# Optimization experiments

Hardware: AMD Instinct MI355X
Metric: run time of the kernel (lower is better)

Reference implementation:

```python
import jax, jax.numpy as jnp
import numpy as np

HID, HEADS, HD = 512, 8, 64  # hid_dim, n_heads, head_dim
NEG = -1e10


def setup_inputs() -> dict:
    key = jax.random.key(0)
    ks = jax.random.split(key, 12)
    B, S = 4, 2048
    inp = {
        'query': jax.random.normal(ks[0], (B, S, HID), jnp.float32),
        'key': jax.random.normal(ks[1], (B, S, HID), jnp.float32),
        'value': jax.random.normal(ks[2], (B, S, HID), jnp.float32),
        'mask': jnp.ones((B, 1, 1, S), jnp.int32),
    }
    sc = 1.0 / np.sqrt(HID)
    for i, n in enumerate(['Wq', 'Wk', 'Wv', 'Wo']):
        inp[n] = jax.random.uniform(ks[3 + i], (HID, HID), jnp.float32, -sc, sc)
    for i, n in enumerate(['bq', 'bk', 'bv', 'bo']):
        inp[n] = jax.random.uniform(ks[7 + i], (HID,), jnp.float32, -sc, sc)
    return inp


def reference(query, key, value, mask, Wq, Wk, Wv, Wo, bq, bk, bv, bo):
    B = query.shape[0]

    def proj(x, W, b):
        # torch Linear: x @ W.T + b; then split heads -> [B, H, S, HD]
        y = jnp.einsum('bsd,ed->bse', x, W) + b
        return y.reshape(B, -1, HEADS, HD).transpose(0, 2, 1, 3)

    Q = proj(query, Wq, bq)
    K = proj(key, Wk, bk)
    V = proj(value, Wv, bv)
    scale = jnp.sqrt(jnp.float32(HD))
    E = jnp.einsum('bhqd,bhkd->bhqk', Q, K) / scale  # [B,H,Sq,Sk]
    E = jnp.where(mask == 0, NEG, E)
    A = jax.nn.softmax(E, axis=-1)  # dropout p=0 -> identity
    out = jnp.einsum('bhqk,bhkd->bhqd', A, V)
    out = out.transpose(0, 2, 1, 3).reshape(B, -1, HID)
    return jnp.einsum('bsd,ed->bse', out, Wo) + bo
```

## Files before the change

kernel.cpp:

```cpp
#include <hip/hip_runtime.h>
#include <hip/hip_bf16.h>


typedef __bf16 v8bf __attribute__((ext_vector_type(8)));
typedef __bf16 v4bf __attribute__((ext_vector_type(4)));
typedef float  v4f  __attribute__((ext_vector_type(4)));

#define MFMA16(a, b, c) __builtin_amdgcn_mfma_f32_16x16x32_bf16((a), (b), (c), 0, 0, 0)

#define QSCALE 0.1803368801111f

__device__ inline v8bf cvt8(const float* __restrict__ p) {
    const v4f f0 = *(const v4f*)p;
    const v4f f1 = *(const v4f*)(p + 4);
    v8bf r;
    r[0] = (__bf16)f0[0]; r[1] = (__bf16)f0[1]; r[2] = (__bf16)f0[2]; r[3] = (__bf16)f0[3];
    r[4] = (__bf16)f1[0]; r[5] = (__bf16)f1[1]; r[6] = (__bf16)f1[2]; r[7] = (__bf16)f1[3];
    return r;
}

__global__ __launch_bounds__(256) void cvt_w(
    const float* __restrict__ Wq, const float* __restrict__ Wk,
    const float* __restrict__ Wv, const float* __restrict__ Wo,
    __bf16* __restrict__ out)
{
    const int idx = (blockIdx.x * 256 + threadIdx.x) * 4;
    const int w = idx >> 18, off = idx & 262143;
    const float* src = (w == 0) ? Wq : (w == 1) ? Wk : (w == 2) ? Wv : Wo;
    const float sc = (w == 0) ? QSCALE : 1.0f;
    const v4f x = *(const v4f*)(src + off);
    v4bf y;
    y[0] = (__bf16)(x[0] * sc); y[1] = (__bf16)(x[1] * sc);
    y[2] = (__bf16)(x[2] * sc); y[3] = (__bf16)(x[3] * sc);
    *(v4bf*)(out + idx) = y;
}

__global__ __launch_bounds__(256) void qkv_gemm(
    const float* __restrict__ xq, const float* __restrict__ xk, const float* __restrict__ xv,
    const __bf16* __restrict__ Wb,
    const float* __restrict__ bq, const float* __restrict__ bk, const float* __restrict__ bv,
    __bf16* __restrict__ Qo, __bf16* __restrict__ Ko, __bf16* __restrict__ VTo)
{
    const int z = blockIdx.z;
    const float*  x    = (z == 0) ? xq : (z == 1) ? xk : xv;
    const __bf16* W    = Wb + (size_t)z * 262144;
    const float*  bias = (z == 0) ? bq : (z == 1) ? bk : bv;
    const float   bsc  = (z == 0) ? QSCALE : 1.0f;

    const int tid = threadIdx.x, wave = tid >> 6, lane = tid & 63;
    const int quad = lane >> 4, r = lane & 15;
    const int wm = wave >> 1, wn = wave & 1;
    const int row0 = blockIdx.x * 128, col0 = blockIdx.y * 128;

    __shared__ __align__(16) __bf16 As[8192];
    __shared__ __align__(16) __bf16 Bs[8192];

    const float*  aptr[4];
    const __bf16* bptr[4];
    int adst[4], bdst[4];
    for (int j = 0; j < 4; j++) {
        const int e = tid + 256 * j;
        const int seg = e >> 6, ln = e & 63;
        aptr[j] = x + (size_t)(row0 + (seg >> 1) * 16 + (ln & 15)) * 512
                    + (seg & 1) * 32 + (ln >> 4) * 8;
        adst[j] = e * 8;
        const int segb = wave * 4 + j;
        bptr[j] = W + (size_t)(col0 + (segb >> 1) * 16 + r) * 512
                    + (segb & 1) * 32 + quad * 8;
        bdst[j] = (segb * 64 + lane) * 8;
    }

    v4f acc[4][4] = {};
    v8bf aReg[4], bReg[4];
    for (int j = 0; j < 4; j++) {
        aReg[j] = cvt8(aptr[j]);
        bReg[j] = *(const v8bf*)bptr[j];
    }

    for (int ki = 0; ki < 8; ki++) {
        __syncthreads();
        for (int j = 0; j < 4; j++) {
            *(v8bf*)&As[adst[j]] = aReg[j];
            *(v8bf*)&Bs[bdst[j]] = bReg[j];
        }
        __syncthreads();
        if (ki < 7) {
            const int kk = (ki + 1) * 64;
            for (int j = 0; j < 4; j++) {
                aReg[j] = cvt8(aptr[j] + kk);
                bReg[j] = *(const v8bf*)(bptr[j] + kk);
            }
        }
        for (int kc = 0; kc < 2; kc++) {
            v8bf a[4], b[4];
            for (int i = 0; i < 4; i++)
                a[i] = ((const v8bf*)As)[((wm * 4 + i) * 2 + kc) * 64 + lane];
            for (int i = 0; i < 4; i++)
                b[i] = ((const v8bf*)Bs)[((wn * 4 + i) * 2 + kc) * 64 + lane];
            for (int mi = 0; mi < 4; mi++)
                for (int ni = 0; ni < 4; ni++)
                    acc[mi][ni] = MFMA16(a[mi], b[ni], acc[mi][ni]);
        }
    }

    for (int ni = 0; ni < 4; ni++) {
        const int n = col0 + wn * 64 + ni * 16 + r;
        const float bv_ = bias[n] * bsc;
        const int hh = n >> 6, hd = n & 63;
        for (int mi = 0; mi < 4; mi++) {
            const int mbase = row0 + wm * 64 + mi * 16 + quad * 4;
            const int bb = mbase >> 11, s0 = mbase & 2047;
            if (z == 2) {
                v4bf pk;
                for (int i = 0; i < 4; i++)
                    pk[i] = (__bf16)(acc[mi][ni][i] + bv_);
                *(v4bf*)&VTo[((size_t)((bb * 8 + hh) * 64 + hd)) * 2048 + s0] = pk;
            } else {
                __bf16* dst = (z == 0) ? Qo : Ko;
                for (int i = 0; i < 4; i++)
                    dst[((size_t)((bb * 8 + hh) * 2048 + s0 + i)) * 64 + hd] =
                        (__bf16)(acc[mi][ni][i] + bv_);
            }
        }
    }
}

__global__ __launch_bounds__(256) void attn(
    const __bf16* __restrict__ Q, const __bf16* __restrict__ K,
    const __bf16* __restrict__ VT, const int* __restrict__ mask,
    __bf16* __restrict__ AO)
{
    const int bh = blockIdx.y, b = bh >> 3, h = bh & 7;
    const int tid = threadIdx.x, wave = tid >> 6, lane = tid & 63;
    const int quad = lane >> 4, r = lane & 15;
    const int q0 = blockIdx.x * 64 + wave * 16;

    const __bf16* Qb = Q  + (size_t)bh * 2048 * 64;
    const __bf16* Kb = K  + (size_t)bh * 2048 * 64;
    const __bf16* Vb = VT + (size_t)bh * 64 * 2048;
    const int*    mb = mask + (size_t)b * 2048;

    __shared__ __align__(16) __bf16 Kls[4096];
    __shared__ __align__(16) __bf16 Vls[4096];
    __shared__ __align__(16) __bf16 Pls[4][16][88];
    __shared__ __bf16 biasLS[2048];

    for (int i = tid; i < 2048; i += 256)
        biasLS[i] = (mb[i] != 0) ? (__bf16)0.f : (__bf16)(-1e10f);

    const int e1 = tid, e2 = tid + 256;
    int seg, l, t_, h_, rr, qd;
    seg = e1 >> 6; l = e1 & 63; t_ = seg >> 1; h_ = seg & 1; rr = l & 15; qd = l >> 4;
    const __bf16* kg1 = Kb + (size_t)(16 * t_ + rr) * 64   + h_ * 32 + qd * 8;
    const __bf16* vg1 = Vb + (size_t)(16 * t_ + rr) * 2048 + h_ * 32 + qd * 8;
    seg = e2 >> 6; l = e2 & 63; t_ = seg >> 1; h_ = seg & 1; rr = l & 15; qd = l >> 4;
    const __bf16* kg2 = Kb + (size_t)(16 * t_ + rr) * 64   + h_ * 32 + qd * 8;
    const __bf16* vg2 = Vb + (size_t)(16 * t_ + rr) * 2048 + h_ * 32 + qd * 8;

    v8bf qf0 = *(const v8bf*)(Qb + (size_t)(q0 + r) * 64 +      quad * 8);
    v8bf qf1 = *(const v8bf*)(Qb + (size_t)(q0 + r) * 64 + 32 + quad * 8);

    v8bf ones;
    for (int i = 0; i < 8; i++) ones[i] = (__bf16)1.0f;

    v4f o[4] = {};
    v4f lacc = {};

    v8bf ks1 = *(const v8bf*)kg1, ks2 = *(const v8bf*)kg2;
    v8bf vs1 = *(const v8bf*)vg1, vs2 = *(const v8bf*)vg2;

    for (int t = 0; t < 32; t++) {
        __syncthreads();
        ((v8bf*)Kls)[e1] = ks1; ((v8bf*)Kls)[e2] = ks2;
        ((v8bf*)Vls)[e1] = vs1; ((v8bf*)Vls)[e2] = vs2;
        __syncthreads();
        if (t < 31) {
            const int k0n = (t + 1) * 64;
            ks1 = *(const v8bf*)(kg1 + (size_t)k0n * 64);
            ks2 = *(const v8bf*)(kg2 + (size_t)k0n * 64);
            vs1 = *(const v8bf*)(vg1 + k0n);
            vs2 = *(const v8bf*)(vg2 + k0n);
        }
        const int k0 = t * 64;

        v4f sa[4] = {};
        for (int tt = 0; tt < 4; tt++) {
            v8bf kf0 = ((const v8bf*)Kls)[(tt * 2 + 0) * 64 + lane];
            v8bf kf1 = ((const v8bf*)Kls)[(tt * 2 + 1) * 64 + lane];
            sa[tt] = MFMA16(kf0, qf0, sa[tt]);
            sa[tt] = MFMA16(kf1, qf1, sa[tt]);
        }

        for (int tt = 0; tt < 4; tt++) {
            const v4bf bl = *(const v4bf*)&biasLS[k0 + tt * 16 + quad * 4];
            v4bf pk;
            for (int i = 0; i < 4; i++)
                pk[i] = (__bf16)exp2f(sa[tt][i] + (float)bl[i]);
            *(v4bf*)&Pls[wave][r][tt * 16 + quad * 4] = pk;
        }
        asm volatile("s_waitcnt lgkmcnt(0)" ::: "memory");
        v8bf pa0 = *(const v8bf*)&Pls[wave][r][     quad * 8];
        v8bf pa1 = *(const v8bf*)&Pls[wave][r][32 + quad * 8];

        lacc = MFMA16(pa0, ones, lacc);
        lacc = MFMA16(pa1, ones, lacc);

        for (int t2 = 0; t2 < 4; t2++) {
            v8bf vf0 = ((const v8bf*)Vls)[(t2 * 2 + 0) * 64 + lane];
            v8bf vf1 = ((const v8bf*)Vls)[(t2 * 2 + 1) * 64 + lane];
            o[t2] = MFMA16(pa0, vf0, o[t2]);
            o[t2] = MFMA16(pa1, vf1, o[t2]);
        }
    }

    for (int t2 = 0; t2 < 4; t2++) {
        const int hd = t2 * 16 + r;
        for (int i = 0; i < 4; i++) {
            const int s = q0 + quad * 4 + i;
            AO[((size_t)b * 2048 + s) * 512 + h * 64 + hd] = (__bf16)(o[t2][i] / lacc[i]);
        }
    }
}

__global__ __launch_bounds__(256) void out_gemm(
    const __bf16* __restrict__ Ai, const __bf16* __restrict__ W,
    const float* __restrict__ bias, float* __restrict__ y)
{
    const int tid = threadIdx.x, wave = tid >> 6, lane = tid & 63;
    const int quad = lane >> 4, r = lane & 15;
    const int wm = wave >> 1, wn = wave & 1;
    const int row0 = blockIdx.x * 128, col0 = blockIdx.y * 128;

    __shared__ __align__(16) __bf16 As[8192];
    __shared__ __align__(16) __bf16 Bs[8192];

    const __bf16* aptr[4];
    const __bf16* bptr[4];
    int dst_[4];
    for (int j = 0; j < 4; j++) {
        const int segb = wave * 4 + j;
        aptr[j] = Ai + (size_t)(row0 + (segb >> 1) * 16 + r) * 512 + (segb & 1) * 32 + quad * 8;
        bptr[j] = W  + (size_t)(col0 + (segb >> 1) * 16 + r) * 512 + (segb & 1) * 32 + quad * 8;
        dst_[j] = (segb * 64 + lane) * 8;
    }

    v4f acc[4][4] = {};
    v8bf aReg[4], bReg[4];
    for (int j = 0; j < 4; j++) {
        aReg[j] = *(const v8bf*)aptr[j];
        bReg[j] = *(const v8bf*)bptr[j];
    }

    for (int ki = 0; ki < 8; ki++) {
        __syncthreads();
        for (int j = 0; j < 4; j++) {
            *(v8bf*)&As[dst_[j]] = aReg[j];
            *(v8bf*)&Bs[dst_[j]] = bReg[j];
        }
        __syncthreads();
        if (ki < 7) {
            const int kk = (ki + 1) * 64;
            for (int j = 0; j < 4; j++) {
                aReg[j] = *(const v8bf*)(aptr[j] + kk);
                bReg[j] = *(const v8bf*)(bptr[j] + kk);
            }
        }
        for (int kc = 0; kc < 2; kc++) {
            v8bf a[4], b[4];
            for (int i = 0; i < 4; i++)
                a[i] = ((const v8bf*)As)[((wm * 4 + i) * 2 + kc) * 64 + lane];
            for (int i = 0; i < 4; i++)
                b[i] = ((const v8bf*)Bs)[((wn * 4 + i) * 2 + kc) * 64 + lane];
            for (int mi = 0; mi < 4; mi++)
                for (int ni = 0; ni < 4; ni++)
                    acc[mi][ni] = MFMA16(a[mi], b[ni], acc[mi][ni]);
        }
    }

    for (int ni = 0; ni < 4; ni++) {
        const int n = col0 + wn * 64 + ni * 16 + r;
        const float bv_ = bias[n];
        for (int mi = 0; mi < 4; mi++) {
            const int mbase = row0 + wm * 64 + mi * 16 + quad * 4;
            for (int i = 0; i < 4; i++)
                y[(size_t)(mbase + i) * 512 + n] = acc[mi][ni][i] + bv_;
        }
    }
}

extern "C" void kernel_launch(void* const* d_in, const int* in_sizes, int n_in,
                              void* d_out, int out_size, void* d_ws, size_t ws_size,
                              hipStream_t stream)
{
    const float* q    = (const float*)d_in[0];
    const float* k    = (const float*)d_in[1];
    const float* v    = (const float*)d_in[2];
    const int*   mask = (const int*)d_in[3];
    const float* Wq   = (const float*)d_in[4];
    const float* Wk   = (const float*)d_in[5];
    const float* Wv   = (const float*)d_in[6];
    const float* Wo   = (const float*)d_in[7];
    const float* bq   = (const float*)d_in[8];
    const float* bk   = (const float*)d_in[9];
    const float* bv   = (const float*)d_in[10];
    const float* bo   = (const float*)d_in[11];

    __bf16* ws  = (__bf16*)d_ws;
    __bf16* Qw  = ws;
    __bf16* Kw  = ws + 4194304;
    __bf16* VTw = ws + 8388608;
    __bf16* AOw = ws + 12582912;
    __bf16* Wb  = ws + 16777216;

    cvt_w<<<dim3(1024), 256, 0, stream>>>(Wq, Wk, Wv, Wo, Wb);
    qkv_gemm<<<dim3(64, 4, 3), 256, 0, stream>>>(q, k, v, Wb, bq, bk, bv, Qw, Kw, VTw);
    attn<<<dim3(32, 32), 256, 0, stream>>>(Qw, Kw, VTw, mask, AOw);
    out_gemm<<<dim3(64, 4), 256, 0, stream>>>(AOw, Wb + 786432, bo, (float*)d_out);
}
```

Measured before the change: 240.4 us.

## Keep attention probabilities in registers and feed PV via 16x16x16 MFMA

Drops the per-wave LDS round-trip for P: the S accumulator layout is reused directly as the B operand of a 16x16x16 bf16 MFMA against a padded V tile in LDS. The mask bias is folded into the QK MFMA accumulator init, and the row sum is computed with scalar adds plus cross-lane shuffles instead of an MFMA against a ones vector. The output is now stored as vectorized 4-wide bf16 writes. In exchange it uses twice as many smaller PV MFMAs and a new V staging layout with 72-element padding.

```diff
diff --git a/kernel.cpp b/kernel.cpp
--- a/kernel.cpp
+++ b/kernel.cpp
@@ -5,8 +5,14 @@
 typedef __bf16 v8bf __attribute__((ext_vector_type(8)));
 typedef __bf16 v4bf __attribute__((ext_vector_type(4)));
 typedef float  v4f  __attribute__((ext_vector_type(4)));
+typedef short  v4s  __attribute__((ext_vector_type(4)));
 
 #define MFMA16(a, b, c) __builtin_amdgcn_mfma_f32_16x16x32_bf16((a), (b), (c), 0, 0, 0)
+
+__device__ inline v4f MFMA_PV(v4bf a, v4bf b, v4f c) {
+    return __builtin_amdgcn_mfma_f32_16x16x16bf16_1k(
+        __builtin_bit_cast(v4s, a), __builtin_bit_cast(v4s, b), c, 0, 0, 0);
+}
 
 #define QSCALE 0.1803368801111f
 
@@ -141,38 +147,39 @@
     const int*    mb = mask + (size_t)b * 2048;
 
     __shared__ __align__(16) __bf16 Kls[4096];
-    __shared__ __align__(16) __bf16 Vls[4096];
-    __shared__ __align__(16) __bf16 Pls[4][16][88];
-    __shared__ __bf16 biasLS[2048];
+    __shared__ __align__(16) __bf16 Vls[64 * 72];
+    __shared__ float biasF[2048];
 
     for (int i = tid; i < 2048; i += 256)
-        biasLS[i] = (mb[i] != 0) ? (__bf16)0.f : (__bf16)(-1e10f);
+        biasF[i] = (mb[i] != 0) ? 0.f : -1e10f;
 
     const int e1 = tid, e2 = tid + 256;
-    int seg, l, t_, h_, rr, qd;
-    seg = e1 >> 6; l = e1 & 63; t_ = seg >> 1; h_ = seg & 1; rr = l & 15; qd = l >> 4;
-    const __bf16* kg1 = Kb + (size_t)(16 * t_ + rr) * 64   + h_ * 32 + qd * 8;
-    const __bf16* vg1 = Vb + (size_t)(16 * t_ + rr) * 2048 + h_ * 32 + qd * 8;
-    seg = e2 >> 6; l = e2 & 63; t_ = seg >> 1; h_ = seg & 1; rr = l & 15; qd = l >> 4;
-    const __bf16* kg2 = Kb + (size_t)(16 * t_ + rr) * 64   + h_ * 32 + qd * 8;
-    const __bf16* vg2 = Vb + (size_t)(16 * t_ + rr) * 2048 + h_ * 32 + qd * 8;
+    int seg, l_, t_, h_, rr, qd;
+    seg = e1 >> 6; l_ = e1 & 63; t_ = seg >> 1; h_ = seg & 1; rr = l_ & 15; qd = l_ >> 4;
+    const __bf16* kg1 = Kb + (size_t)(16 * t_ + rr) * 64 + h_ * 32 + qd * 8;
+    seg = e2 >> 6; l_ = e2 & 63; t_ = seg >> 1; h_ = seg & 1; rr = l_ & 15; qd = l_ >> 4;
+    const __bf16* kg2 = Kb + (size_t)(16 * t_ + rr) * 64 + h_ * 32 + qd * 8;
+
+    const int hd1 = tid >> 3, c1 = tid & 7;
+    const __bf16* vg1 = Vb + (size_t)hd1 * 2048 + c1 * 8;
+    const __bf16* vg2 = Vb + (size_t)(hd1 + 32) * 2048 + c1 * 8;
+    const int dV1 = hd1 * 72 + c1 * 8, dV2 = (hd1 + 32) * 72 + c1 * 8;
 
     v8bf qf0 = *(const v8bf*)(Qb + (size_t)(q0 + r) * 64 +      quad * 8);
     v8bf qf1 = *(const v8bf*)(Qb + (size_t)(q0 + r) * 64 + 32 + quad * 8);
 
-    v8bf ones;
-    for (int i = 0; i < 8; i++) ones[i] = (__bf16)1.0f;
-
+    float ssum = 0.f;
     v4f o[4] = {};
-    v4f lacc = {};
 
     v8bf ks1 = *(const v8bf*)kg1, ks2 = *(const v8bf*)kg2;
     v8bf vs1 = *(const v8bf*)vg1, vs2 = *(const v8bf*)vg2;
 
+    const int vbase = r * 72 + quad * 4;
+
     for (int t = 0; t < 32; t++) {
         __syncthreads();
         ((v8bf*)Kls)[e1] = ks1; ((v8bf*)Kls)[e2] = ks2;
-        ((v8bf*)Vls)[e1] = vs1; ((v8bf*)Vls)[e2] = vs2;
+        *(v8bf*)&Vls[dV1] = vs1; *(v8bf*)&Vls[dV2] = vs2;
         __syncthreads();
         if (t < 31) {
             const int k0n = (t + 1) * 64;
@@ -183,42 +190,41 @@
         }
         const int k0 = t * 64;
 
-        v4f sa[4] = {};
+        v4f sa[4];
         for (int tt = 0; tt < 4; tt++) {
+            const v4f bias4 = *(const v4f*)&biasF[k0 + tt * 16 + quad * 4];
             v8bf kf0 = ((const v8bf*)Kls)[(tt * 2 + 0) * 64 + lane];
             v8bf kf1 = ((const v8bf*)Kls)[(tt * 2 + 1) * 64 + lane];
-            sa[tt] = MFMA16(kf0, qf0, sa[tt]);
+            sa[tt] = MFMA16(kf0, qf0, bias4);
             sa[tt] = MFMA16(kf1, qf1, sa[tt]);
         }
 
+        v4bf pf[4];
         for (int tt = 0; tt < 4; tt++) {
-            const v4bf bl = *(const v4bf*)&biasLS[k0 + tt * 16 + quad * 4];
-            v4bf pk;
-            for (int i = 0; i < 4; i++)
-                pk[i] = (__bf16)exp2f(sa[tt][i] + (float)bl[i]);
-            *(v4bf*)&Pls[wave][r][tt * 16 + quad * 4] = pk;
-        }
-        asm volatile("s_waitcnt lgkmcnt(0)" ::: "memory");
-        v8bf pa0 = *(const v8bf*)&Pls[wave][r][     quad * 8];
-        v8bf pa1 = *(const v8bf*)&Pls[wave][r][32 + quad * 8];
-
-        lacc = MFMA16(pa0, ones, lacc);
-        lacc = MFMA16(pa1, ones, lacc);
-
-        for (int t2 = 0; t2 < 4; t2++) {
-            v8bf vf0 = ((const v8bf*)Vls)[(t2 * 2 + 0) * 64 + lane];
-            v8bf vf1 = ((const v8bf*)Vls)[(t2 * 2 + 1) * 64 + lane];
-            o[t2] = MFMA16(pa0, vf0, o[t2]);
-            o[t2] = MFMA16(pa1, vf1, o[t2]);
-        }
-    }
-
+            for (int i = 0; i < 4; i++) {
+                const float p = exp2f(sa[tt][i]);
+                ssum += p;
+                pf[tt][i] = (__bf16)p;
+            }
+        }
+
+        for (int g = 0; g < 4; g++)
+            for (int t2 = 0; t2 < 4; t2++) {
+                const v4bf vf = *(const v4bf*)&Vls[t2 * 1152 + vbase + g * 16];
+                o[t2] = MFMA_PV(vf, pf[g], o[t2]);
+            }
+    }
+
+    ssum += __shfl_xor(ssum, 16);
+    ssum += __shfl_xor(ssum, 32);
+    const float inv = 1.0f / ssum;
+
+    __bf16* dst = AO + ((size_t)b * 2048 + q0 + r) * 512 + h * 64 + quad * 4;
     for (int t2 = 0; t2 < 4; t2++) {
-        const int hd = t2 * 16 + r;
-        for (int i = 0; i < 4; i++) {
-            const int s = q0 + quad * 4 + i;
-            AO[((size_t)b * 2048 + s) * 512 + h * 64 + hd] = (__bf16)(o[t2][i] / lacc[i]);
-        }
+        v4bf pk;
+        for (int i = 0; i < 4; i++)
+            pk[i] = (__bf16)(o[t2][i] * inv);
+        *(v4bf*)(dst + t2 * 16) = pk;
     }
 }
 
```

Measured after the change: 239.9 us. No clear change (-0.2%).
